# Kernel tuning notes

Hardware: AMD Instinct MI355X
Metric: run time of the kernel (lower is better)

Reference implementation:

```python
import jax, jax.numpy as jnp
import numpy as np

EMB = 1024
HEAD = 16
DK = 64
DV = 64
B, SQ, SKV_FULL = 4, 2048, 2048
SPLIT_RATIO = 0.5
SKV = int(SKV_FULL * SPLIT_RATIO)  # rank-0 keeps first half of KV


def setup_inputs() -> dict:
    key = jax.random.key(0)
    ks = jax.random.split(key, 10)
    s = 0.02
    x_q = jax.random.normal(ks[0], (B, SQ, EMB), jnp.float32)
    x_k_v = jax.random.normal(ks[1], (B, SKV_FULL, EMB), jnp.float32)
    attn_mask = jax.random.randint(ks[2], (B, SQ, SKV), 0, 2) > 0
    # nn.Linear params: weight [out, in], bias [out]
    w_q_w = jax.random.normal(ks[3], (HEAD * DK, EMB), jnp.float32) * s
    w_q_b = jax.random.normal(ks[4], (HEAD * DK,), jnp.float32) * s
    w_k_w = jax.random.normal(ks[5], (HEAD * DK, EMB), jnp.float32) * s
    w_k_b = jax.random.normal(ks[6], (HEAD * DK,), jnp.float32) * s
    w_v_w = jax.random.normal(ks[7], (HEAD * DV, EMB), jnp.float32) * s
    w_v_b = jax.random.normal(ks[8], (HEAD * DV,), jnp.float32) * s
    return {"x_q": x_q, "x_k_v": x_k_v, "attn_mask": attn_mask,
            "w_q_w": w_q_w, "w_q_b": w_q_b, "w_k_w": w_k_w, "w_k_b": w_k_b,
            "w_v_w": w_v_w, "w_v_b": w_v_b}


def reference(x_q, x_k_v, attn_mask, w_q_w, w_q_b, w_k_w, w_k_b, w_v_w, w_v_b):
    q = x_q @ w_q_w.T + w_q_b            # [B, SQ, H*DK]
    k = x_k_v @ w_k_w.T + w_k_b          # [B, SKV_FULL, H*DK]
    v = x_k_v @ w_v_w.T + w_v_b          # [B, SKV_FULL, H*DV]
    # rank-0 kv_cache keeps only the first split_idx positions, detached
    split_idx = int(k.shape[1] * SPLIT_RATIO)
    k = jax.lax.stop_gradient(k[:, :split_idx])
    v = jax.lax.stop_gradient(v[:, :split_idx])
    qh = q.reshape(B, SQ, HEAD, DK).transpose(0, 2, 1, 3)    # [B,H,SQ,DK]
    kh = k.reshape(B, SKV, HEAD, DK).transpose(0, 2, 1, 3)   # [B,H,SKV,DK]
    vh = v.reshape(B, SKV, HEAD, DV).transpose(0, 2, 1, 3)   # [B,H,SKV,DV]
    attn = jnp.einsum('bhqd,bhkd->bhqk', qh, kh) / jnp.sqrt(jnp.float32(DK))
    attn = jnp.where(attn_mask[:, None, :, :], jnp.float32(-1e9), attn)
    attn = jax.nn.softmax(attn, axis=-1)
    z = jnp.einsum('bhqk,bhkd->bhqd', attn, vh)              # [B,H,SQ,DV]
    return z.transpose(0, 2, 1, 3).reshape(B, SQ, HEAD * DV)
```

## Files before the change

### kernel.cpp

```cpp
#include <hip/hip_runtime.h>
#include <hip/hip_bf16.h>

typedef __hip_bfloat16 bf16;
typedef __attribute__((ext_vector_type(8))) short bf16x8;
typedef __attribute__((ext_vector_type(4))) float f32x4;

#define EMB 1024
#define HEADS 16
#define DKV 64
#define SQL 2048
#define SKVL 1024

#define QSCALE 0.1803368801111204f

__device__ __forceinline__ f32x4 mfma16(bf16x8 a, bf16x8 b, f32x4 c) {
  return __builtin_amdgcn_mfma_f32_16x16x32_bf16(a, b, c, 0, 0, 0);
}

__device__ __forceinline__ void gload16(const void* g, void* l) {
  __builtin_amdgcn_global_load_lds((const __attribute__((address_space(1))) void*)g,
                                   (__attribute__((address_space(3))) void*)l,
                                   16, 0, 0);
}

__device__ __forceinline__ short to_bf16s(float f) {
  bf16 h = __float2bfloat16(f);
  return *reinterpret_cast<short*>(&h);
}

__device__ __forceinline__ void cvt_store(bf16* dst, int i, float4 v) {
  short4 o;
  o.x = to_bf16s(v.x); o.y = to_bf16s(v.y); o.z = to_bf16s(v.z); o.w = to_bf16s(v.w);
  reinterpret_cast<short4*>(dst)[i] = o;
}

__global__ __launch_bounds__(256) void k_convall(
    const float* __restrict__ xq, const float* __restrict__ xkv,
    const float* __restrict__ wq, const float* __restrict__ wk,
    const float* __restrict__ wv,
    bf16* __restrict__ xq_b, bf16* __restrict__ xkv_b,
    bf16* __restrict__ wq_b, bf16* __restrict__ wk_b, bf16* __restrict__ wv_b) {
  int i = blockIdx.x * 256 + threadIdx.x;
  if (i < 2097152) {
    cvt_store(xq_b, i, reinterpret_cast<const float4*>(xq)[i]);
  } else if (i < 3145728) {
    int j = i - 2097152;
    int row = j >> 8, c4 = j & 255;
    int b = row >> 10, s = row & 1023;
    cvt_store(xkv_b, j, reinterpret_cast<const float4*>(xkv)[((b << 11) + s) * 256 + c4]);
  } else if (i < 3407872) {
    int j = i - 3145728;
    cvt_store(wq_b, j, reinterpret_cast<const float4*>(wq)[j]);
  } else if (i < 3670016) {
    int j = i - 3407872;
    cvt_store(wk_b, j, reinterpret_cast<const float4*>(wk)[j]);
  } else {
    int j = i - 3670016;
    cvt_store(wv_b, j, reinterpret_cast<const float4*>(wv)[j]);
  }
}

__global__ __launch_bounds__(256) void k_pack(const int* __restrict__ m,
                                              unsigned* __restrict__ out) {
  int i = blockIdx.x * 256 + threadIdx.x;
  unsigned long long bm = __ballot(m[i] != 0);
  int lane = threadIdx.x & 63;
  if ((lane & 31) == 0) out[i >> 5] = (unsigned)(bm >> (lane & 32));
}

template<int MODE>
__device__ void gemm_body(const bf16* __restrict__ A, const bf16* __restrict__ W,
                          const float* __restrict__ bias, bf16* __restrict__ out,
                          bf16* As, bf16* Bs) {
  const int tid = threadIdx.x;
  const int lane = tid & 63;
  const int wid = tid >> 6;
  const int wm = wid >> 1, wn = wid & 1;
  const int bm = blockIdx.x * 128;
  const int bn = blockIdx.y * 128;

  f32x4 acc[4][4] = {};

  const int r0 = wid * 16 + (lane >> 2);
  const int ke = (lane & 3) * 8;
  const bf16* a0 = A + (long)(bm + r0) * EMB + ke;
  const bf16* a1 = a0 + 64 * EMB;
  const bf16* w0 = W + (long)(bn + r0) * EMB + ke;
  const bf16* w1 = w0 + 64 * EMB;
  char* lA0 = (char*)As + wid * 1024;
  char* lA1 = (char*)As + (4 + wid) * 1024;
  char* lB0 = (char*)Bs + wid * 1024;
  char* lB1 = (char*)Bs + (4 + wid) * 1024;

  const int frow = lane & 15;
  const int fkb = (lane >> 4) * 16;
  const char* pa = (const char*)As + (wm * 64 + frow) * 64 + fkb;
  const char* pb = (const char*)Bs + (wn * 64 + frow) * 64 + fkb;

  for (int k0 = 0; k0 < EMB; k0 += 32) {
    __syncthreads();
    gload16(a0 + k0, lA0);
    gload16(a1 + k0, lA1);
    gload16(w0 + k0, lB0);
    gload16(w1 + k0, lB1);
    __syncthreads();
    bf16x8 af[4], bfr[4];
#pragma unroll
    for (int i = 0; i < 4; ++i) af[i] = *(const bf16x8*)(pa + i * 16 * 64);
#pragma unroll
    for (int j = 0; j < 4; ++j) bfr[j] = *(const bf16x8*)(pb + j * 16 * 64);
#pragma unroll
    for (int i = 0; i < 4; ++i)
#pragma unroll
      for (int j = 0; j < 4; ++j)
        acc[i][j] = (MODE == 2) ? mfma16(bfr[j], af[i], acc[i][j])
                                : mfma16(af[i], bfr[j], acc[i][j]);
  }

  const int g4 = (lane >> 4) * 4;
#pragma unroll
  for (int i = 0; i < 4; ++i)
#pragma unroll
    for (int j = 0; j < 4; ++j)
#pragma unroll
      for (int r = 0; r < 4; ++r) {
        if (MODE != 2) {
          int mrow = bm + wm * 64 + i * 16 + g4 + r;
          int ncol = bn + wn * 64 + j * 16 + frow;
          float v = acc[i][j][r] + bias[ncol];
          int hh = ncol >> 6, d = ncol & 63;
          long idx;
          if (MODE == 0) {
            v *= QSCALE;
            int b = mrow >> 11, s = mrow & 2047;
            idx = ((long)(b * HEADS + hh) * SQL + s) * DKV + d;
          } else {
            int b = mrow >> 10, s = mrow & 1023;
            idx = ((long)(b * HEADS + hh) * SKVL + s) * DKV + d;
          }
          out[idx] = __float2bfloat16(v);
        } else {
          int nrow = bn + wn * 64 + j * 16 + g4 + r;
          int mcol = bm + wm * 64 + i * 16 + frow;
          float v = acc[i][j][r] + bias[nrow];
          int hh = nrow >> 6, d = nrow & 63;
          int b = mcol >> 10, s = mcol & 1023;
          long idx = ((long)(b * HEADS + hh) * DKV + d) * SKVL + s;
          out[idx] = __float2bfloat16(v);
        }
      }
}

__global__ __launch_bounds__(256) void k_gemm3(
    const bf16* __restrict__ xq, const bf16* __restrict__ xkv,
    const bf16* __restrict__ wq, const bf16* __restrict__ wk,
    const bf16* __restrict__ wv,
    const float* __restrict__ bq, const float* __restrict__ bk,
    const float* __restrict__ bv,
    bf16* __restrict__ Qb, bf16* __restrict__ Kb, bf16* __restrict__ Vtb) {
  __shared__ __align__(16) bf16 As[128 * 32];
  __shared__ __align__(16) bf16 Bs[128 * 32];
  int mode = blockIdx.z;
  if (mode == 0) {
    gemm_body<0>(xq, wq, bq, Qb, As, Bs);
  } else if (mode == 1) {
    if (blockIdx.x >= 32) return;
    gemm_body<1>(xkv, wk, bk, Kb, As, Bs);
  } else {
    if (blockIdx.x >= 32) return;
    gemm_body<2>(xkv, wv, bv, Vtb, As, Bs);
  }
}

__global__ __launch_bounds__(256) void k_attn(const bf16* __restrict__ Q,
                                              const bf16* __restrict__ Kc,
                                              const bf16* __restrict__ Vt,
                                              const unsigned* __restrict__ mp,
                                              float* __restrict__ out) {
  __shared__ __align__(16) bf16 Ks[64 * 64];
  __shared__ __align__(16) bf16 Vs[64 * 64];
  __shared__ __align__(16) bf16 Ps[4][16 * 64];
  const int tid = threadIdx.x, lane = tid & 63, wid = tid >> 6;
  const int bh = blockIdx.y;
  const int b = bh >> 4, h = bh & 15;
  const int qw = blockIdx.x * 64 + wid * 16;

  const int frow = lane & 15;
  const int fkb = (lane >> 4) * 16;
  const int g4 = (lane >> 4) * 4;

  const bf16* qp = Q + ((long)bh * SQL + qw + frow) * DKV + (lane >> 4) * 8;
  bf16x8 qf0 = *(const bf16x8*)qp;
  bf16x8 qf1 = *(const bf16x8*)(qp + 32);

  const uint2* mrp = (const uint2*)(mp + ((long)b * SQL + qw + frow) * 32);

  const int srow = tid >> 3;
  const int sinn = ((tid & 7) * 16) ^ ((srow & 7) << 4);
  const char* kgb = (const char*)Kc + ((long)bh * SKVL + srow) * 128 + sinn;
  const char* vgb = (const char*)Vt + ((long)bh * DKV + srow) * 2048 + sinn;

  f32x4 zacc[4] = {};
  float mrow = -3e38f;
  float lrow = 0.f;

  uint4 kr0 = *(const uint4*)(kgb);
  uint4 kr1 = *(const uint4*)(kgb + 32 * 128);
  uint4 vr0 = *(const uint4*)(vgb);
  uint4 vr1 = *(const uint4*)(vgb + 32 * 2048);

  for (int t = 0; t < 16; ++t) {
    __syncthreads();
    *(uint4*)((char*)Ks + tid * 16) = kr0;
    *(uint4*)((char*)Ks + 4096 + tid * 16) = kr1;
    *(uint4*)((char*)Vs + tid * 16) = vr0;
    *(uint4*)((char*)Vs + 4096 + tid * 16) = vr1;
    __syncthreads();
    if (t < 15) {
      kr0 = *(const uint4*)(kgb + (long)(t + 1) * 8192);
      kr1 = *(const uint4*)(kgb + (long)(t + 1) * 8192 + 32 * 128);
      vr0 = *(const uint4*)(vgb + (t + 1) * 128);
      vr1 = *(const uint4*)(vgb + (t + 1) * 128 + 32 * 2048);
    }

    f32x4 s[4];
    __builtin_amdgcn_s_setprio(1);
#pragma unroll
    for (int nj = 0; nj < 4; ++nj) {
      int krow = nj * 16 + frow;
      const char* kb = (const char*)Ks + krow * 128;
      int sw = (krow & 7) << 4;
      bf16x8 kf0 = *(const bf16x8*)(kb + (fkb ^ sw));
      bf16x8 kf1 = *(const bf16x8*)(kb + ((64 + fkb) ^ sw));
      f32x4 sa = {};
      sa = mfma16(kf0, qf0, sa);
      sa = mfma16(kf1, qf1, sa);
      s[nj] = sa;
    }
    __builtin_amdgcn_s_setprio(0);

    uint2 mw = mrp[t];
#pragma unroll
    for (int nj = 0; nj < 4; ++nj) {
      unsigned wmask = (nj < 2) ? mw.x : mw.y;
#pragma unroll
      for (int r = 0; r < 4; ++r) {
        if ((wmask >> (((nj & 1) << 4) + g4 + r)) & 1u) s[nj][r] = -1e9f;
      }
    }

    float tm = s[0][0];
#pragma unroll
    for (int nj = 0; nj < 4; ++nj)
#pragma unroll
      for (int r = 0; r < 4; ++r) tm = fmaxf(tm, s[nj][r]);

    if (__any(tm > mrow + 8.0f)) {
      float tmax = fmaxf(tm, __shfl_xor(tm, 16));
      tmax = fmaxf(tmax, __shfl_xor(tmax, 32));
      float mnew = fmaxf(mrow, tmax);
      float sc = __builtin_amdgcn_exp2f(mrow - mnew);
      mrow = mnew;
      lrow *= sc;
      float scq[4];
#pragma unroll
      for (int r = 0; r < 4; ++r) scq[r] = __shfl(sc, g4 + r);
#pragma unroll
      for (int nj = 0; nj < 4; ++nj)
#pragma unroll
        for (int r = 0; r < 4; ++r) zacc[nj][r] *= scq[r];
    }

    float pr[4][4];
    float psum = 0.f;
#pragma unroll
    for (int nj = 0; nj < 4; ++nj)
#pragma unroll
      for (int r = 0; r < 4; ++r) {
        float e = __builtin_amdgcn_exp2f(s[nj][r] - mrow);
        pr[nj][r] = e;
        psum += e;
      }
    lrow += psum;

    char* pw = (char*)Ps[wid] + frow * 128;
    const int swz = (frow & 7) << 4;
#pragma unroll
    for (int nj = 0; nj < 4; ++nj) {
      short4 pk;
      pk.x = to_bf16s(pr[nj][0]);
      pk.y = to_bf16s(pr[nj][1]);
      pk.z = to_bf16s(pr[nj][2]);
      pk.w = to_bf16s(pr[nj][3]);
      *(short4*)(pw + ((nj * 32 + g4 * 2) ^ swz)) = pk;
    }

    bf16x8 pf0 = *(const bf16x8*)(pw + (fkb ^ swz));
    bf16x8 pf1 = *(const bf16x8*)(pw + ((64 + fkb) ^ swz));
    __builtin_amdgcn_s_setprio(1);
#pragma unroll
    for (int nj = 0; nj < 4; ++nj) {
      int vrow = nj * 16 + frow;
      const char* vb = (const char*)Vs + vrow * 128;
      int swv = (vrow & 7) << 4;
      bf16x8 vf0 = *(const bf16x8*)(vb + (fkb ^ swv));
      bf16x8 vf1 = *(const bf16x8*)(vb + ((64 + fkb) ^ swv));
      zacc[nj] = mfma16(pf0, vf0, zacc[nj]);
      zacc[nj] = mfma16(pf1, vf1, zacc[nj]);
    }
    __builtin_amdgcn_s_setprio(0);
  }

  lrow += __shfl_xor(lrow, 16);
  lrow += __shfl_xor(lrow, 32);
  float invl = 1.0f / lrow;
  float inv[4];
#pragma unroll
  for (int r = 0; r < 4; ++r) inv[r] = __shfl(invl, g4 + r);

#pragma unroll
  for (int r = 0; r < 4; ++r) {
    int q = qw + g4 + r;
#pragma unroll
    for (int nj = 0; nj < 4; ++nj) {
      long idx = ((long)b * SQL + q) * (HEADS * DKV) + h * DKV + nj * 16 + frow;
      out[idx] = zacc[nj][r] * inv[r];
    }
  }
}

extern "C" void kernel_launch(void* const* d_in, const int* in_sizes, int n_in,
                              void* d_out, int out_size, void* d_ws, size_t ws_size,
                              hipStream_t stream) {
  const float* x_q = (const float*)d_in[0];
  const float* x_kv = (const float*)d_in[1];
  const int* mask = (const int*)d_in[2];
  const float* wqw = (const float*)d_in[3];
  const float* wqb = (const float*)d_in[4];
  const float* wkw = (const float*)d_in[5];
  const float* wkb = (const float*)d_in[6];
  const float* wvw = (const float*)d_in[7];
  const float* wvb = (const float*)d_in[8];
  float* out = (float*)d_out;

  char* w = (char*)d_ws;
  bf16* xq_b  = (bf16*)(w);
  bf16* xkv_b = (bf16*)(w + (16l << 20));
  bf16* wq_b  = (bf16*)(w + (24l << 20));
  bf16* wk_b  = (bf16*)(w + (26l << 20));
  bf16* wv_b  = (bf16*)(w + (28l << 20));
  bf16* Qb    = (bf16*)(w + (30l << 20));
  bf16* Kb    = (bf16*)(w + (46l << 20));
  bf16* Vtb   = (bf16*)(w + (54l << 20));
  unsigned* mpk = (unsigned*)(w + (62l << 20));

  k_convall<<<15360, 256, 0, stream>>>(x_q, x_kv, wqw, wkw, wvw,
                                       xq_b, xkv_b, wq_b, wk_b, wv_b);
  k_pack<<<32768, 256, 0, stream>>>(mask, mpk);
  k_gemm3<<<dim3(64, 8, 3), 256, 0, stream>>>(xq_b, xkv_b, wq_b, wk_b, wv_b,
                                              wqb, wkb, wvb, Qb, Kb, Vtb);
  k_attn<<<dim3(32, 64), 256, 0, stream>>>(Qb, Kb, Vtb, mpk, out);
}
```

Measured before the change: 274.0 us.

## Switch attention to 32x32x16 MFMA with register-resident P via permlane swap

Restructures the attention kernel so each wave handles 32 query rows with 32x32x16 bf16 MFMA instead of 16x16x32. The softmax probabilities stay in registers: they are packed with v_cvt_pk_bf16_f32 and rearranged with v_permlane32_swap, which removes the LDS round-trip through the per-wave P buffer. Each block now covers 128 queries, so the grid halves, and launch bounds request 3 blocks per CU. In exchange, register pressure rises with 16-wide accumulators, and occupancy may drop.

```diff
diff --git a/kernel.cpp b/kernel.cpp
--- a/kernel.cpp
+++ b/kernel.cpp
@@ -4,6 +4,7 @@
 typedef __hip_bfloat16 bf16;
 typedef __attribute__((ext_vector_type(8))) short bf16x8;
 typedef __attribute__((ext_vector_type(4))) float f32x4;
+typedef __attribute__((ext_vector_type(16))) float f32x16;
 
 #define EMB 1024
 #define HEADS 16
@@ -16,6 +17,9 @@
 __device__ __forceinline__ f32x4 mfma16(bf16x8 a, bf16x8 b, f32x4 c) {
   return __builtin_amdgcn_mfma_f32_16x16x32_bf16(a, b, c, 0, 0, 0);
 }
+__device__ __forceinline__ f32x16 mfma32(bf16x8 a, bf16x8 b, f32x16 c) {
+  return __builtin_amdgcn_mfma_f32_32x32x16_bf16(a, b, c, 0, 0, 0);
+}
 
 __device__ __forceinline__ void gload16(const void* g, void* l) {
   __builtin_amdgcn_global_load_lds((const __attribute__((address_space(1))) void*)g,
@@ -26,6 +30,12 @@
 __device__ __forceinline__ short to_bf16s(float f) {
   bf16 h = __float2bfloat16(f);
   return *reinterpret_cast<short*>(&h);
+}
+
+__device__ __forceinline__ unsigned cvtpk_bf16(float lo, float hi) {
+  unsigned r;
+  asm("v_cvt_pk_bf16_f32 %0, %1, %2" : "=v"(r) : "v"(lo), "v"(hi));
+  return r;
 }
 
 __device__ __forceinline__ void cvt_store(bf16* dst, int i, float4 v) {
@@ -172,35 +182,35 @@
   }
 }
 
-__global__ __launch_bounds__(256) void k_attn(const bf16* __restrict__ Q,
-                                              const bf16* __restrict__ Kc,
-                                              const bf16* __restrict__ Vt,
-                                              const unsigned* __restrict__ mp,
-                                              float* __restrict__ out) {
+__global__ __launch_bounds__(256, 3) void k_attn(const bf16* __restrict__ Q,
+                                                 const bf16* __restrict__ Kc,
+                                                 const bf16* __restrict__ Vt,
+                                                 const unsigned* __restrict__ mp,
+                                                 float* __restrict__ out) {
   __shared__ __align__(16) bf16 Ks[64 * 64];
   __shared__ __align__(16) bf16 Vs[64 * 64];
-  __shared__ __align__(16) bf16 Ps[4][16 * 64];
   const int tid = threadIdx.x, lane = tid & 63, wid = tid >> 6;
   const int bh = blockIdx.y;
-  const int b = bh >> 4, h = bh & 15;
-  const int qw = blockIdx.x * 64 + wid * 16;
-
-  const int frow = lane & 15;
-  const int fkb = (lane >> 4) * 16;
-  const int g4 = (lane >> 4) * 4;
-
-  const bf16* qp = Q + ((long)bh * SQL + qw + frow) * DKV + (lane >> 4) * 8;
-  bf16x8 qf0 = *(const bf16x8*)qp;
-  bf16x8 qf1 = *(const bf16x8*)(qp + 32);
-
-  const uint2* mrp = (const uint2*)(mp + ((long)b * SQL + qw + frow) * 32);
+  const int b = bh >> 4, hd = bh & 15;
+  const int qw = blockIdx.x * 128 + wid * 32;
+  const int l31 = lane & 31;
+  const int hh = lane >> 5;
+  const int q_lane = qw + l31;
+  const int swzA = (l31 & 7) << 4;
+
+  const char* qrow = (const char*)Q + ((long)bh * SQL + q_lane) * 128 + hh * 16;
+  bf16x8 qf[4];
+#pragma unroll
+  for (int kt = 0; kt < 4; ++kt) qf[kt] = *(const bf16x8*)(qrow + kt * 32);
+
+  const uint2* mrp = (const uint2*)(mp + ((long)b * SQL + q_lane) * 32);
 
   const int srow = tid >> 3;
   const int sinn = ((tid & 7) * 16) ^ ((srow & 7) << 4);
   const char* kgb = (const char*)Kc + ((long)bh * SKVL + srow) * 128 + sinn;
   const char* vgb = (const char*)Vt + ((long)bh * DKV + srow) * 2048 + sinn;
 
-  f32x4 zacc[4] = {};
+  f32x16 zacc0 = {}, zacc1 = {};
   float mrow = -3e38f;
   float lrow = 0.f;
 
@@ -208,6 +218,11 @@
   uint4 kr1 = *(const uint4*)(kgb + 32 * 128);
   uint4 vr0 = *(const uint4*)(vgb);
   uint4 vr1 = *(const uint4*)(vgb + 32 * 2048);
+
+  const char* KsC = (const char*)Ks;
+  const char* VsC = (const char*)Vs;
+  const int kb0 = l31 * 128;
+  const int kb1 = kb0 + 4096;
 
   for (int t = 0; t < 16; ++t) {
     __syncthreads();
@@ -223,109 +238,94 @@
       vr1 = *(const uint4*)(vgb + (t + 1) * 128 + 32 * 2048);
     }
 
-    f32x4 s[4];
+    f32x16 s0 = {}, s1 = {};
     __builtin_amdgcn_s_setprio(1);
 #pragma unroll
-    for (int nj = 0; nj < 4; ++nj) {
-      int krow = nj * 16 + frow;
-      const char* kb = (const char*)Ks + krow * 128;
-      int sw = (krow & 7) << 4;
-      bf16x8 kf0 = *(const bf16x8*)(kb + (fkb ^ sw));
-      bf16x8 kf1 = *(const bf16x8*)(kb + ((64 + fkb) ^ sw));
-      f32x4 sa = {};
-      sa = mfma16(kf0, qf0, sa);
-      sa = mfma16(kf1, qf1, sa);
-      s[nj] = sa;
+    for (int m = 0; m < 4; ++m) {
+      int off = (m * 32 + hh * 16) ^ swzA;
+      bf16x8 kf0 = *(const bf16x8*)(KsC + kb0 + off);
+      bf16x8 kf1 = *(const bf16x8*)(KsC + kb1 + off);
+      s0 = mfma32(kf0, qf[m], s0);
+      s1 = mfma32(kf1, qf[m], s1);
     }
     __builtin_amdgcn_s_setprio(0);
 
     uint2 mw = mrp[t];
-#pragma unroll
-    for (int nj = 0; nj < 4; ++nj) {
-      unsigned wmask = (nj < 2) ? mw.x : mw.y;
-#pragma unroll
-      for (int r = 0; r < 4; ++r) {
-        if ((wmask >> (((nj & 1) << 4) + g4 + r)) & 1u) s[nj][r] = -1e9f;
-      }
-    }
-
-    float tm = s[0][0];
-#pragma unroll
-    for (int nj = 0; nj < 4; ++nj)
-#pragma unroll
-      for (int r = 0; r < 4; ++r) tm = fmaxf(tm, s[nj][r]);
+    unsigned w0s = mw.x >> (hh << 2);
+    unsigned w1s = mw.y >> (hh << 2);
+#pragma unroll
+    for (int r = 0; r < 16; ++r) {
+      const int BR = (r & 3) + 8 * (r >> 2);
+      if ((w0s >> BR) & 1u) s0[r] = -1e9f;
+      if ((w1s >> BR) & 1u) s1[r] = -1e9f;
+    }
+
+    float tm = fmaxf(s0[0], s1[0]);
+#pragma unroll
+    for (int r = 1; r < 16; ++r) tm = fmaxf(tm, fmaxf(s0[r], s1[r]));
 
     if (__any(tm > mrow + 8.0f)) {
-      float tmax = fmaxf(tm, __shfl_xor(tm, 16));
-      tmax = fmaxf(tmax, __shfl_xor(tmax, 32));
+      float tmax = fmaxf(tm, __shfl_xor(tm, 32));
       float mnew = fmaxf(mrow, tmax);
       float sc = __builtin_amdgcn_exp2f(mrow - mnew);
       mrow = mnew;
       lrow *= sc;
-      float scq[4];
-#pragma unroll
-      for (int r = 0; r < 4; ++r) scq[r] = __shfl(sc, g4 + r);
-#pragma unroll
-      for (int nj = 0; nj < 4; ++nj)
-#pragma unroll
-        for (int r = 0; r < 4; ++r) zacc[nj][r] *= scq[r];
-    }
-
-    float pr[4][4];
-    float psum = 0.f;
-#pragma unroll
-    for (int nj = 0; nj < 4; ++nj)
-#pragma unroll
-      for (int r = 0; r < 4; ++r) {
-        float e = __builtin_amdgcn_exp2f(s[nj][r] - mrow);
-        pr[nj][r] = e;
-        psum += e;
+#pragma unroll
+      for (int r = 0; r < 16; ++r) {
+        const int BR = (r & 3) + 8 * (r >> 2);
+        float scr = __shfl(sc, (BR + 4 * hh) | (lane & 32));
+        zacc0[r] *= scr;
+        zacc1[r] *= scr;
       }
-    lrow += psum;
-
-    char* pw = (char*)Ps[wid] + frow * 128;
-    const int swz = (frow & 7) << 4;
-#pragma unroll
-    for (int nj = 0; nj < 4; ++nj) {
-      short4 pk;
-      pk.x = to_bf16s(pr[nj][0]);
-      pk.y = to_bf16s(pr[nj][1]);
-      pk.z = to_bf16s(pr[nj][2]);
-      pk.w = to_bf16s(pr[nj][3]);
-      *(short4*)(pw + ((nj * 32 + g4 * 2) ^ swz)) = pk;
-    }
-
-    bf16x8 pf0 = *(const bf16x8*)(pw + (fkb ^ swz));
-    bf16x8 pf1 = *(const bf16x8*)(pw + ((64 + fkb) ^ swz));
+    }
+
+    float psA = 0.f, psB = 0.f;
+#pragma unroll
+    for (int r = 0; r < 16; ++r) {
+      float p0 = __builtin_amdgcn_exp2f(s0[r] - mrow);
+      float p1 = __builtin_amdgcn_exp2f(s1[r] - mrow);
+      s0[r] = p0; s1[r] = p1;
+      psA += p0; psB += p1;
+    }
+    lrow += psA + psB;
+
     __builtin_amdgcn_s_setprio(1);
 #pragma unroll
-    for (int nj = 0; nj < 4; ++nj) {
-      int vrow = nj * 16 + frow;
-      const char* vb = (const char*)Vs + vrow * 128;
-      int swv = (vrow & 7) << 4;
-      bf16x8 vf0 = *(const bf16x8*)(vb + (fkb ^ swv));
-      bf16x8 vf1 = *(const bf16x8*)(vb + ((64 + fkb) ^ swv));
-      zacc[nj] = mfma16(pf0, vf0, zacc[nj]);
-      zacc[nj] = mfma16(pf1, vf1, zacc[nj]);
+    for (int kt = 0; kt < 4; ++kt) {
+      const int gA = 2 * kt, gB = 2 * kt + 1;
+      const int bA = 4 * (gA & 3), bB = 4 * (gB & 3);
+      float a0f, a1f, a2f, a3f, b0f, b1f, b2f, b3f;
+      if (gA < 4) { a0f = s0[bA]; a1f = s0[bA + 1]; a2f = s0[bA + 2]; a3f = s0[bA + 3]; }
+      else        { a0f = s1[bA]; a1f = s1[bA + 1]; a2f = s1[bA + 2]; a3f = s1[bA + 3]; }
+      if (gB < 4) { b0f = s0[bB]; b1f = s0[bB + 1]; b2f = s0[bB + 2]; b3f = s0[bB + 3]; }
+      else        { b0f = s1[bB]; b1f = s1[bB + 1]; b2f = s1[bB + 2]; b3f = s1[bB + 3]; }
+      unsigned pa0 = cvtpk_bf16(a0f, a1f);
+      unsigned pa1 = cvtpk_bf16(a2f, a3f);
+      unsigned pb0 = cvtpk_bf16(b0f, b1f);
+      unsigned pb1 = cvtpk_bf16(b2f, b3f);
+      asm("v_permlane32_swap_b32 %0, %1" : "+v"(pa0), "+v"(pb0));
+      asm("v_permlane32_swap_b32 %0, %1" : "+v"(pa1), "+v"(pb1));
+      uint4 pu = {pa0, pa1, pb0, pb1};
+      bf16x8 pfrag = __builtin_bit_cast(bf16x8, pu);
+      int off = (kt * 32 + hh * 16) ^ swzA;
+      bf16x8 vf0 = *(const bf16x8*)(VsC + kb0 + off);
+      bf16x8 vf1 = *(const bf16x8*)(VsC + kb1 + off);
+      zacc0 = mfma32(pfrag, vf0, zacc0);
+      zacc1 = mfma32(pfrag, vf1, zacc1);
     }
     __builtin_amdgcn_s_setprio(0);
   }
 
-  lrow += __shfl_xor(lrow, 16);
   lrow += __shfl_xor(lrow, 32);
   float invl = 1.0f / lrow;
-  float inv[4];
-#pragma unroll
-  for (int r = 0; r < 4; ++r) inv[r] = __shfl(invl, g4 + r);
-
-#pragma unroll
-  for (int r = 0; r < 4; ++r) {
-    int q = qw + g4 + r;
-#pragma unroll
-    for (int nj = 0; nj < 4; ++nj) {
-      long idx = ((long)b * SQL + q) * (HEADS * DKV) + h * DKV + nj * 16 + frow;
-      out[idx] = zacc[nj][r] * inv[r];
-    }
+#pragma unroll
+  for (int r = 0; r < 16; ++r) {
+    const int BR = (r & 3) + 8 * (r >> 2);
+    float invr = __shfl(invl, (BR + 4 * hh) | (lane & 32));
+    int q = qw + BR + 4 * hh;
+    long base = ((long)b * SQL + q) * (HEADS * DKV) + hd * DKV + l31;
+    out[base] = zacc0[r] * invr;
+    out[base + 32] = zacc1[r] * invr;
   }
 }
 
@@ -359,5 +359,5 @@
   k_pack<<<32768, 256, 0, stream>>>(mask, mpk);
   k_gemm3<<<dim3(64, 8, 3), 256, 0, stream>>>(xq_b, xkv_b, wq_b, wk_b, wv_b,
                                               wqb, wkb, wvb, Qb, Kb, Vtb);
-  k_attn<<<dim3(32, 64), 256, 0, stream>>>(Qb, Kb, Vtb, mpk, out);
-}
+  k_attn<<<dim3(16, 64), 256, 0, stream>>>(Qb, Kb, Vtb, mpk, out);
+}
```

After: 265.1 us. 1.03x faster.
